# Performance work log

Hardware: AMD Instinct MI355X
Metric: run time of the kernel (lower is better)

The kernel has to match this reference:

```python
import jax, jax.numpy as jnp
import numpy as np

N_PATCHES = 256
PATCH = 16
D = 768
H = 12
DH = D // H
L = 12
OUT_D = 10
EPS = 1e-5


def _pos_embed(seq_len, d):
    i = np.arange(seq_len)[:, None].astype(np.float64)
    j = np.arange(d)[None, :].astype(np.float64)
    angle_even = i / 10000 ** (j / d)
    angle_odd = i / 10000 ** ((j - 1) / d)
    pe = np.where(np.arange(d)[None, :] % 2 == 0, np.sin(angle_even), np.cos(angle_odd))
    return jnp.asarray(pe, dtype=jnp.float32)


def _layernorm(x, g, b):
    mu = jnp.mean(x, axis=-1, keepdims=True)
    var = jnp.var(x, axis=-1, keepdims=True)
    return (x - mu) * jax.lax.rsqrt(var + EPS) * g + b


def setup_inputs() -> dict:
    key = jax.random.key(0)
    ks = jax.random.split(key, 16)
    s = 0.02
    return {
        "images": jax.random.normal(ks[0], (64, 1, N_PATCHES * PATCH), dtype=jnp.float32),
        "Wemb": jax.random.normal(ks[1], (D, PATCH), dtype=jnp.float32) * s,
        "bemb": jnp.zeros((D,), jnp.float32),
        "cls": jax.random.uniform(ks[2], (1, D), dtype=jnp.float32),
        "Wq": jax.random.normal(ks[3], (L, H, DH, DH), dtype=jnp.float32) * s,
        "bq": jnp.zeros((L, H, DH), jnp.float32),
        "Wk": jax.random.normal(ks[4], (L, H, DH, DH), dtype=jnp.float32) * s,
        "bk": jnp.zeros((L, H, DH), jnp.float32),
        "Wv": jax.random.normal(ks[5], (L, H, DH, DH), dtype=jnp.float32) * s,
        "bv": jnp.zeros((L, H, DH), jnp.float32),
        "ln1_g": jnp.ones((L, D), jnp.float32),
        "ln1_b": jnp.zeros((L, D), jnp.float32),
        "ln2_g": jnp.ones((L, D), jnp.float32),
        "ln2_b": jnp.zeros((L, D), jnp.float32),
        "W1": jax.random.normal(ks[6], (L, 4 * D, D), dtype=jnp.float32) * s,
        "b1": jnp.zeros((L, 4 * D), jnp.float32),
        "W2": jax.random.normal(ks[7], (L, D, 4 * D), dtype=jnp.float32) * s,
        "b2": jnp.zeros((L, D), jnp.float32),
        "Whead": jax.random.normal(ks[8], (OUT_D, D), dtype=jnp.float32) * s,
        "bhead": jnp.zeros((OUT_D,), jnp.float32),
    }


def reference(images, Wemb, bemb, cls, Wq, bq, Wk, bk, Wv, bv,
              ln1_g, ln1_b, ln2_g, ln2_b, W1, b1, W2, b2, Whead, bhead):
    n = images.shape[0]
    # patchify: (N,1,Lspec) -> (N, n_patches, patch_size)
    patches = images.reshape(n, N_PATCHES, PATCH)
    tok = jnp.einsum("npi,di->npd", patches, Wemb) + bemb  # linear embed
    tok = jnp.concatenate([jnp.broadcast_to(cls[None], (n, 1, D)), tok], axis=1)
    tok = tok + _pos_embed(N_PATCHES + 1, D)[None]  # (N, S, D), S = 257

    scale = 1.0 / jnp.sqrt(jnp.float32(DH))
    for l in range(L):
        x = tok
        h = _layernorm(x, ln1_g[l], ln1_b[l]).reshape(n, -1, H, DH)
        q = jnp.einsum("nshd,hod->nsho", h, Wq[l]) + bq[l][None, None]
        k = jnp.einsum("nshd,hod->nsho", h, Wk[l]) + bk[l][None, None]
        v = jnp.einsum("nshd,hod->nsho", h, Wv[l]) + bv[l][None, None]
        att = jax.nn.softmax(jnp.einsum("nqho,nkho->nhqk", q, k) * scale, axis=-1)
        o = jnp.einsum("nhqk,nkho->nqho", att, v).reshape(n, -1, D)
        x = x + o  # residual (no output projection in original MSA)
        h2 = _layernorm(x, ln2_g[l], ln2_b[l])
        mlp = jax.nn.gelu(jnp.einsum("nsd,fd->nsf", h2, W1[l]) + b1[l], approximate=False)
        tok = x + jnp.einsum("nsf,df->nsd", mlp, W2[l]) + b2[l]

    logits = tok[:, 0] @ Whead.T + bhead
    return jax.nn.softmax(logits, axis=-1)
```

## Files before the change

kernel.cpp:

```cpp
#include <hip/hip_runtime.h>
#include <math.h>
#include <stdint.h>

#define N_IMG 64
#define S_LEN 257
#define D_MODEL 768
#define H_HEADS 12
#define L_LAYERS 12
#define F_HID 3072
#define OUT_DIM 10
#define R_ROWS (N_IMG * S_LEN)
#define R_PAD 16640
#define SKV 320

typedef unsigned short ushort_t;
typedef __attribute__((ext_vector_type(4))) float f32x4;
typedef __attribute__((ext_vector_type(8))) short short8;
typedef __attribute__((ext_vector_type(2))) unsigned int u32x2;

__device__ __forceinline__ ushort_t f2bf(float x) {
    unsigned u = __float_as_uint(x);
    u += 0x7fffu + ((u >> 16) & 1u);
    return (ushort_t)(u >> 16);
}
__device__ __forceinline__ unsigned pack2(float a, float b) {
    return (unsigned)f2bf(a) | ((unsigned)f2bf(b) << 16);
}

__device__ __forceinline__ void glds16(const ushort_t* g, const ushort_t* l) {
    __builtin_amdgcn_global_load_lds(
        (const __attribute__((address_space(1))) unsigned int*)(uintptr_t)g,
        (__attribute__((address_space(3))) unsigned int*)(uintptr_t)l,
        16, 0, 0);
}

__global__ __launch_bounds__(256) void pos_kernel(float* __restrict__ pos) {
    int i = blockIdx.x;
    int t = threadIdx.x;
    for (int u = 0; u < 3; ++u) {
        int j = t + 256 * u;
        double e = (double)(j & ~1) / 768.0;
        double angle = (double)i * exp(-e * 9.210340371976184);
        double v = (j & 1) ? cos(angle) : sin(angle);
        pos[i * 768 + j] = (float)v;
    }
}

__global__ __launch_bounds__(256) void embed_kernel(const float* __restrict__ images,
                                                    const float* __restrict__ Wemb,
                                                    const float* __restrict__ bemb,
                                                    const float* __restrict__ cls,
                                                    const float* __restrict__ pos,
                                                    float* __restrict__ tok) {
    int b = blockIdx.x;
    int n = b / S_LEN, s = b % S_LEN;
    int t = threadIdx.x;
    __shared__ float p[16];
    if (s > 0 && t < 16) p[t] = images[n * 4096 + (s - 1) * 16 + t];
    __syncthreads();
    for (int u = 0; u < 3; ++u) {
        int d = t + 256 * u;
        float acc;
        if (s == 0) {
            acc = cls[d];
        } else {
            acc = bemb[d];
            const float4* w = (const float4*)(Wemb + d * 16);
            float4 w0 = w[0], w1 = w[1], w2 = w[2], w3 = w[3];
            acc += p[0] * w0.x + p[1] * w0.y + p[2] * w0.z + p[3] * w0.w;
            acc += p[4] * w1.x + p[5] * w1.y + p[6] * w1.z + p[7] * w1.w;
            acc += p[8] * w2.x + p[9] * w2.y + p[10] * w2.z + p[11] * w2.w;
            acc += p[12] * w3.x + p[13] * w3.y + p[14] * w3.z + p[15] * w3.w;
        }
        tok[(size_t)b * 768 + d] = acc + pos[s * 768 + d];
    }
}

__global__ __launch_bounds__(256) void ln_kernel(const float* __restrict__ x,
                                                 const float* __restrict__ g,
                                                 const float* __restrict__ b,
                                                 ushort_t* __restrict__ y) {
    int row = blockIdx.x * 4 + (threadIdx.x >> 6);
    int lane = threadIdx.x & 63;
    const float* xr = x + (size_t)row * 768 + lane * 4;
    float4 a0 = *(const float4*)xr;
    float4 a1 = *(const float4*)(xr + 256);
    float4 a2 = *(const float4*)(xr + 512);
    float s = (a0.x + a0.y + a0.z + a0.w) + (a1.x + a1.y + a1.z + a1.w) + (a2.x + a2.y + a2.z + a2.w);
    float sq = a0.x*a0.x + a0.y*a0.y + a0.z*a0.z + a0.w*a0.w
             + a1.x*a1.x + a1.y*a1.y + a1.z*a1.z + a1.w*a1.w
             + a2.x*a2.x + a2.y*a2.y + a2.z*a2.z + a2.w*a2.w;
    for (int o = 32; o; o >>= 1) {
        s += __shfl_xor(s, o);
        sq += __shfl_xor(sq, o);
    }
    float mu = s * (1.0f / 768.0f);
    float var = sq * (1.0f / 768.0f) - mu * mu;
    float rs = rsqrtf(var + 1e-5f);
    ushort_t* yr = y + (size_t)row * 768 + lane * 4;
#pragma unroll
    for (int i = 0; i < 3; ++i) {
        float4 av = (i == 0) ? a0 : (i == 1) ? a1 : a2;
        const float4 gg = *(const float4*)(g + lane * 4 + i * 256);
        const float4 bb = *(const float4*)(b + lane * 4 + i * 256);
        float o0 = (av.x - mu) * rs * gg.x + bb.x;
        float o1 = (av.y - mu) * rs * gg.y + bb.y;
        float o2 = (av.z - mu) * rs * gg.z + bb.z;
        float o3 = (av.w - mu) * rs * gg.w + bb.w;
        *(u32x2*)(yr + i * 256) = (u32x2){pack2(o0, o1), pack2(o2, o3)};
    }
}

__global__ __launch_bounds__(256) void conv_layer(const float* __restrict__ Wq,
                                                  const float* __restrict__ Wk,
                                                  const float* __restrict__ Wv,
                                                  const float* __restrict__ W1l,
                                                  const float* __restrict__ W2l,
                                                  ushort_t* __restrict__ wqkvbf,
                                                  ushort_t* __restrict__ w1bf,
                                                  ushort_t* __restrict__ w2bf) {
    const int NQKV = H_HEADS * 192 * 64;
    const int NW = F_HID * D_MODEL;
    int idx = (blockIdx.x * 256 + threadIdx.x) * 4;
    if (idx < NQKV) {
        int h = idx / (192 * 64);
        int rem = idx - h * 192 * 64;
        int o3 = rem >> 6, d = rem & 63;
        const float* src;
        int o;
        if (o3 < 64)       { src = Wq; o = o3; }
        else if (o3 < 128) { src = Wk; o = o3 - 64; }
        else               { src = Wv; o = o3 - 128; }
        float4 v = *(const float4*)(src + ((size_t)(h * 64 + o)) * 64 + d);
        *(u32x2*)(wqkvbf + idx) = (u32x2){pack2(v.x, v.y), pack2(v.z, v.w)};
    } else if (idx < NQKV + NW) {
        int i = idx - NQKV;
        float4 v = *(const float4*)(W1l + i);
        *(u32x2*)(w1bf + i) = (u32x2){pack2(v.x, v.y), pack2(v.z, v.w)};
    } else {
        int i = idx - NQKV - NW;
        float4 v = *(const float4*)(W2l + i);
        *(u32x2*)(w2bf + i) = (u32x2){pack2(v.x, v.y), pack2(v.z, v.w)};
    }
}

__global__ __launch_bounds__(256) void qkv_mfma(const ushort_t* __restrict__ xbf,
                                                const ushort_t* __restrict__ wqkv,
                                                const float* __restrict__ bq,
                                                const float* __restrict__ bk,
                                                const float* __restrict__ bv,
                                                ushort_t* __restrict__ qhb,
                                                ushort_t* __restrict__ khb,
                                                ushort_t* __restrict__ vtb) {
    __shared__ ushort_t As[128 * 64];
    int rt = blockIdx.x;
    int h = blockIdx.y;
    int t = threadIdx.x, lane = t & 63, wid = t >> 6;
    int wr = wid >> 1, wc = wid & 1;
    {
        int lr = t >> 3, lg = t & 7;
#pragma unroll
        for (int u = 0; u < 4; ++u) {
            int r = u * 32 + lr;
            int grow = rt * 128 + r;
            if (grow >= R_ROWS) grow = R_ROWS - 1;
            short8 a = *(const short8*)(xbf + (size_t)grow * 768 + h * 64 + lg * 8);
            *(short8*)&As[r * 64 + (lg ^ (r & 7)) * 8] = a;
        }
    }
    __syncthreads();
    int frow = lane & 15, g = lane >> 4;
    const ushort_t* wb = wqkv + (size_t)h * (192 * 64);
    f32x4 acc[4][6];
#pragma unroll
    for (int m = 0; m < 4; ++m)
#pragma unroll
        for (int n = 0; n < 6; ++n) acc[m][n] = (f32x4){0.f, 0.f, 0.f, 0.f};
#pragma unroll
    for (int kk = 0; kk < 2; ++kk) {
        short8 af[4], bfr[6];
#pragma unroll
        for (int m = 0; m < 4; ++m) {
            int r = wr * 64 + m * 16 + frow;
            af[m] = *(const short8*)&As[r * 64 + ((kk * 4 + g) ^ (r & 7)) * 8];
        }
#pragma unroll
        for (int n = 0; n < 6; ++n)
            bfr[n] = *(const short8*)(wb + (size_t)(wc * 96 + n * 16 + frow) * 64 + kk * 32 + g * 8);
#pragma unroll
        for (int m = 0; m < 4; ++m)
#pragma unroll
            for (int n = 0; n < 6; ++n)
                acc[m][n] = __builtin_amdgcn_mfma_f32_16x16x32_bf16(bfr[n], af[m], acc[m][n], 0, 0, 0);
    }
#pragma unroll
    for (int m = 0; m < 4; ++m) {
        int token = rt * 128 + wr * 64 + m * 16 + frow;
        if (token < R_ROWS) {
            unsigned nimg = (unsigned)token / 257u;
            unsigned s = (unsigned)token - nimg * 257u;
            size_t qk_base = ((size_t)(nimg * H_HEADS + h) * 257 + s) * 64;
            size_t v_base = (size_t)(nimg * H_HEADS + h) * (64 * SKV);
#pragma unroll
            for (int n = 0; n < 6; ++n) {
                int c = wc * 96 + n * 16 + g * 4;
                f32x4 a = acc[m][n];
                if (c < 64) {
                    const float4 bb = *(const float4*)(bq + h * 64 + c);
                    *(u32x2*)(qhb + qk_base + c) = (u32x2){
                        pack2((a[0] + bb.x) * 0.125f, (a[1] + bb.y) * 0.125f),
                        pack2((a[2] + bb.z) * 0.125f, (a[3] + bb.w) * 0.125f)};
                } else if (c < 128) {
                    const float4 bb = *(const float4*)(bk + h * 64 + (c - 64));
                    *(u32x2*)(khb + qk_base + (c - 64)) = (u32x2){
                        pack2(a[0] + bb.x, a[1] + bb.y), pack2(a[2] + bb.z, a[3] + bb.w)};
                } else {
                    const float4 bb = *(const float4*)(bv + h * 64 + (c - 128));
                    vtb[v_base + (size_t)(c - 128 + 0) * SKV + s] = f2bf(a[0] + bb.x);
                    vtb[v_base + (size_t)(c - 128 + 1) * SKV + s] = f2bf(a[1] + bb.y);
                    vtb[v_base + (size_t)(c - 128 + 2) * SKV + s] = f2bf(a[2] + bb.z);
                    vtb[v_base + (size_t)(c - 128 + 3) * SKV + s] = f2bf(a[3] + bb.w);
                }
            }
        }
    }
}

template <int NST>
__global__ __launch_bounds__(256) void attn_mfma(const ushort_t* __restrict__ qh,
                                                 const ushort_t* __restrict__ kh,
                                                 const ushort_t* __restrict__ vT,
                                                 float* __restrict__ tok, int base) {
    __shared__ ushort_t Plds[4][NST][1024];
    int nh = blockIdx.x;
    int h = nh % H_HEADS, n = nh / H_HEADS;
    int t = threadIdx.x, w = t >> 6, lane = t & 63;
    int lq = lane & 15, g = lane >> 4;
    const size_t hoff = ((size_t)n * H_HEADS + h) * (S_LEN * 64);
    const ushort_t* qhp = qh + hoff;
    const ushort_t* khp = kh + hoff;
    const ushort_t* vp  = vT + ((size_t)n * H_HEADS + h) * (64 * SKV);
    const int xorm = (lq & 7) << 4;

    short8 qf[NST][2];
    int qr0[NST];
    float m[NST], lsum[NST];
    f32x4 o[NST][4];
#pragma unroll
    for (int s = 0; s < NST; ++s) {
        int qrow = base + s * 64 + w * 16 + lq;
        qr0[s] = qrow;
        int qcl = qrow > 256 ? 256 : qrow;
#pragma unroll
        for (int kk = 0; kk < 2; ++kk)
            qf[s][kk] = *(const short8*)(qhp + (size_t)qcl * 64 + kk * 32 + g * 8);
        m[s] = -INFINITY; lsum[s] = 0.f;
#pragma unroll
        for (int dt = 0; dt < 4; ++dt) o[s][dt] = (f32x4){0.f, 0.f, 0.f, 0.f};
    }

    for (int kt = 0; kt < 5; ++kt) {
        short8 ah[4][2];
#pragma unroll
        for (int st = 0; st < 4; ++st) {
            int key = kt * 64 + st * 16 + lq;
            int kcl = key > 256 ? 256 : key;
            const ushort_t* krh = khp + (size_t)kcl * 64 + g * 8;
            ah[st][0] = *(const short8*)krh;
            ah[st][1] = *(const short8*)(krh + 32);
        }
        f32x4 c[NST][4];
#pragma unroll
        for (int s = 0; s < NST; ++s)
#pragma unroll
            for (int st = 0; st < 4; ++st) {
                c[s][st] = (f32x4){0.f, 0.f, 0.f, 0.f};
#pragma unroll
                for (int kk = 0; kk < 2; ++kk)
                    c[s][st] = __builtin_amdgcn_mfma_f32_16x16x32_bf16(ah[st][kk], qf[s][kk], c[s][st], 0, 0, 0);
            }
        float scale[NST];
        unsigned pw[NST][4][2];
#pragma unroll
        for (int s = 0; s < NST; ++s) {
            float tmax = -INFINITY;
#pragma unroll
            for (int st = 0; st < 4; ++st)
#pragma unroll
                for (int j = 0; j < 4; ++j) {
                    int key = kt * 64 + st * 16 + g * 4 + j;
                    float sv = (key <= 256) ? c[s][st][j] : -INFINITY;
                    c[s][st][j] = sv;
                    tmax = fmaxf(tmax, sv);
                }
            tmax = fmaxf(tmax, __shfl_xor(tmax, 16));
            tmax = fmaxf(tmax, __shfl_xor(tmax, 32));
            float mn = fmaxf(m[s], tmax);
            scale[s] = __expf(m[s] - mn);
            float psum = 0.f;
#pragma unroll
            for (int st = 0; st < 4; ++st) {
                float p0 = __expf(c[s][st][0] - mn), p1 = __expf(c[s][st][1] - mn);
                float p2 = __expf(c[s][st][2] - mn), p3 = __expf(c[s][st][3] - mn);
                psum += (p0 + p1) + (p2 + p3);
                pw[s][st][0] = pack2(p0, p1);
                pw[s][st][1] = pack2(p2, p3);
            }
            psum += __shfl_xor(psum, 16);
            psum += __shfl_xor(psum, 32);
            lsum[s] = lsum[s] * scale[s] + psum;
            m[s] = mn;
        }
#pragma unroll
        for (int s = 0; s < NST; ++s) {
            char* pwave = (char*)&Plds[w][s][0];
#pragma unroll
            for (int st = 0; st < 4; ++st) {
                int off = (lq * 128 + st * 32 + g * 8) ^ xorm;
                *(u32x2*)(pwave + off) = (u32x2){pw[s][st][0], pw[s][st][1]};
            }
#pragma unroll
            for (int dt = 0; dt < 4; ++dt) {
                o[s][dt][0] *= scale[s]; o[s][dt][1] *= scale[s];
                o[s][dt][2] *= scale[s]; o[s][dt][3] *= scale[s];
            }
        }
#pragma unroll
        for (int kk = 0; kk < 2; ++kk) {
            short8 pf[NST];
#pragma unroll
            for (int s = 0; s < NST; ++s) {
                int roff = (lq * 128 + kk * 64 + g * 16) ^ xorm;
                pf[s] = *(const short8*)((char*)&Plds[w][s][0] + roff);
            }
#pragma unroll
            for (int dt = 0; dt < 4; ++dt) {
                short8 vf = *(const short8*)(vp + (size_t)(dt * 16 + lq) * SKV + kt * 64 + kk * 32 + g * 8);
#pragma unroll
                for (int s = 0; s < NST; ++s)
                    o[s][dt] = __builtin_amdgcn_mfma_f32_16x16x32_bf16(vf, pf[s], o[s][dt], 0, 0, 0);
            }
        }
    }
#pragma unroll
    for (int s = 0; s < NST; ++s) {
        if (qr0[s] < S_LEN) {
            float inv = 1.0f / lsum[s];
            float* trow = tok + ((size_t)n * S_LEN + qr0[s]) * 768 + h * 64 + g * 4;
#pragma unroll
            for (int dt = 0; dt < 4; ++dt) {
                float4 old = *(const float4*)(trow + dt * 16);
                old.x += o[s][dt][0] * inv;
                old.y += o[s][dt][1] * inv;
                old.z += o[s][dt][2] * inv;
                old.w += o[s][dt][3] * inv;
                *(float4*)(trow + dt * 16) = old;
            }
        }
    }
}

__device__ __forceinline__ float gelu_fast(float x) {
    float s = fabsf(x) * 0.70710678118654752f;
    float t = 1.0f / (1.0f + 0.3275911f * s);
    float y = t * (0.254829592f + t * (-0.284496736f + t * (1.421413741f +
              t * (-1.453152027f + t * 1.061405429f))));
    float erfa = 1.0f - y * __expf(-s * s);
    float erfv = copysignf(erfa, x);
    return 0.5f * x * (1.0f + erfv);
}

template <int MODE>
__global__ __launch_bounds__(512, 2) void mfma_gemm(const ushort_t* __restrict__ A,
                                                    const ushort_t* __restrict__ B,
                                                    const float* __restrict__ bias,
                                                    void* __restrict__ Cv,
                                                    int K, int lda, int ldb, int ldc, int nbn) {
    __shared__ ushort_t As[4][256 * 32];
    __shared__ ushort_t Bs[4][256 * 32];
    int nwg = gridDim.x;
    int orig = blockIdx.x;
    int xcd = orig & 7, idx = orig >> 3;
    int q8 = nwg >> 3, r8 = nwg & 7;
    int cbase = (xcd < r8) ? xcd * (q8 + 1) : r8 * (q8 + 1) + (xcd - r8) * q8;
    int swz = cbase + idx;
    int bm = swz / nbn, bn = swz - bm * nbn;

    int t = threadIdx.x;
    int lane = t & 63, w = t >> 6;
    int wr = w >> 2, wc = w & 3;
    const ushort_t* Ag = A + (size_t)(bm * 256) * lda;
    const ushort_t* Bg = B + (size_t)(bn * 256) * ldb;
    int frow = lane & 15, g = lane >> 4;
    int srow = lane >> 2;
    int scol = ((lane & 3) ^ ((lane >> 3) & 3)) * 8;
    int rslot = (frow >> 1) & 3;

    f32x4 acc[8][4];
#pragma unroll
    for (int m = 0; m < 8; ++m)
#pragma unroll
        for (int n = 0; n < 4; ++n) acc[m][n] = (f32x4){0.f, 0.f, 0.f, 0.f};

    auto STAGE = [&](int buf, int kt) {
        int k0 = kt * 32;
#pragma unroll
        for (int i = 0; i < 2; ++i) {
            int rbase = w * 32 + i * 16;
            glds16(Ag + (size_t)(rbase + srow) * lda + k0 + scol, &As[buf][rbase * 32]);
            glds16(Bg + (size_t)(rbase + srow) * ldb + k0 + scol, &Bs[buf][rbase * 32]);
        }
    };
    STAGE(0, 0);
    STAGE(1, 1);
    STAGE(2, 2);
    int nt = K >> 5;
    for (int it = 0; it < nt; ++it) {
        int ahead = nt - 1 - it;
        if (ahead >= 2)      asm volatile("s_waitcnt vmcnt(8)" ::: "memory");
        else if (ahead == 1) asm volatile("s_waitcnt vmcnt(4)" ::: "memory");
        else                 asm volatile("s_waitcnt vmcnt(0)" ::: "memory");
        asm volatile("s_barrier" ::: "memory");
        if (it + 3 < nt) STAGE((it + 3) & 3, it + 3);
        const ushort_t* Ab = &As[it & 3][0];
        const ushort_t* Bb = &Bs[it & 3][0];
        short8 af[8], bf[4];
#pragma unroll
        for (int m = 0; m < 8; ++m) {
            int r = wr * 128 + m * 16 + frow;
            af[m] = *(const short8*)&Ab[r * 32 + ((g ^ rslot) * 8)];
        }
#pragma unroll
        for (int n = 0; n < 4; ++n) {
            int r = wc * 64 + n * 16 + frow;
            bf[n] = *(const short8*)&Bb[r * 32 + ((g ^ rslot) * 8)];
        }
#pragma unroll
        for (int m = 0; m < 8; ++m)
#pragma unroll
            for (int n = 0; n < 4; ++n)
                acc[m][n] = __builtin_amdgcn_mfma_f32_16x16x32_bf16(bf[n], af[m], acc[m][n], 0, 0, 0);
    }
    int row0 = bm * 256 + wr * 128 + frow;
    int col0 = bn * 256 + wc * 64 + g * 4;
#pragma unroll
    for (int n = 0; n < 4; ++n) {
        int col = col0 + n * 16;
        float4 bb = {0.f, 0.f, 0.f, 0.f};
        if (bias) bb = *(const float4*)(bias + col);
#pragma unroll
        for (int m = 0; m < 8; ++m) {
            int row = row0 + m * 16;
            f32x4 a = acc[m][n];
            float v0 = a[0] + bb.x, v1 = a[1] + bb.y, v2 = a[2] + bb.z, v3 = a[3] + bb.w;
            if (MODE == 0) {
                v0 = gelu_fast(v0); v1 = gelu_fast(v1); v2 = gelu_fast(v2); v3 = gelu_fast(v3);
                *(u32x2*)((ushort_t*)Cv + (size_t)row * ldc + col) =
                    (u32x2){pack2(v0, v1), pack2(v2, v3)};
            } else {
                float* cp = (float*)Cv + (size_t)row * ldc + col;
                float4 old = *(const float4*)cp;
                old.x += v0; old.y += v1; old.z += v2; old.w += v3;
                *(float4*)cp = old;
            }
        }
    }
}

__global__ __launch_bounds__(64) void head_kernel(const float* __restrict__ tok,
                                                  const float* __restrict__ Whead,
                                                  const float* __restrict__ bhead,
                                                  float* __restrict__ out) {
    int n = blockIdx.x;
    int t = threadIdx.x;
    __shared__ float logits[OUT_DIM];
    if (t < OUT_DIM) {
        float acc = bhead[t];
        const float* xr = tok + (size_t)n * S_LEN * 768;
        const float* w = Whead + t * 768;
        for (int d = 0; d < 768; ++d) acc += xr[d] * w[d];
        logits[t] = acc;
    }
    __syncthreads();
    if (t == 0) {
        float m = -INFINITY;
        for (int o = 0; o < OUT_DIM; ++o) m = fmaxf(m, logits[o]);
        float ssum = 0.f;
        float e[OUT_DIM];
        for (int o = 0; o < OUT_DIM; ++o) { e[o] = expf(logits[o] - m); ssum += e[o]; }
        float inv = 1.0f / ssum;
        for (int o = 0; o < OUT_DIM; ++o) out[n * OUT_DIM + o] = e[o] * inv;
    }
}

extern "C" void kernel_launch(void* const* d_in, const int* in_sizes, int n_in,
                              void* d_out, int out_size, void* d_ws, size_t ws_size,
                              hipStream_t stream) {
    const float* images = (const float*)d_in[0];
    const float* Wemb   = (const float*)d_in[1];
    const float* bemb   = (const float*)d_in[2];
    const float* cls    = (const float*)d_in[3];
    const float* Wq     = (const float*)d_in[4];
    const float* bq     = (const float*)d_in[5];
    const float* Wk     = (const float*)d_in[6];
    const float* bk     = (const float*)d_in[7];
    const float* Wv     = (const float*)d_in[8];
    const float* bv     = (const float*)d_in[9];
    const float* ln1_g  = (const float*)d_in[10];
    const float* ln1_b  = (const float*)d_in[11];
    const float* ln2_g  = (const float*)d_in[12];
    const float* ln2_b  = (const float*)d_in[13];
    const float* W1     = (const float*)d_in[14];
    const float* b1     = (const float*)d_in[15];
    const float* W2     = (const float*)d_in[16];
    const float* b2     = (const float*)d_in[17];
    const float* Whead  = (const float*)d_in[18];
    const float* bhead  = (const float*)d_in[19];
    float* out = (float*)d_out;

    const size_t TOKP = (size_t)R_PAD * D_MODEL;
    const size_t QKSZ = (size_t)N_IMG * H_HEADS * S_LEN * 64;
    const size_t VTSZ = (size_t)N_IMG * H_HEADS * 64 * SKV;
    const size_t WSZ  = (size_t)F_HID * D_MODEL;
    float* ws   = (float*)d_ws;
    float* pos  = ws;
    float* tok  = pos + 197376;
    ushort_t* xbf  = (ushort_t*)(tok + TOKP);
    ushort_t* qhb  = xbf + TOKP;
    ushort_t* khb  = qhb + QKSZ;
    ushort_t* vtb  = khb + QKSZ;
    ushort_t* wqkvbf = vtb + VTSZ;
    ushort_t* w1bf = wqkvbf + H_HEADS * 192 * 64;
    ushort_t* w2bf = w1bf + WSZ;
    ushort_t* hid_full = w2bf + WSZ;

    const size_t hid_bytes = (size_t)R_PAD * F_HID * 2;
    const size_t needed = ((char*)hid_full - (char*)d_ws) + hid_bytes;
    int nchunk = (ws_size >= needed) ? 1 : 2;
    int FC = F_HID / nchunk;
    ushort_t* hid = (nchunk == 1) ? hid_full : qhb;

    pos_kernel<<<S_LEN, 256, 0, stream>>>(pos);
    embed_kernel<<<R_ROWS, 256, 0, stream>>>(images, Wemb, bemb, cls, pos, tok);

    for (int l = 0; l < L_LAYERS; ++l) {
        const size_t wqkv_off = (size_t)l * H_HEADS * 64 * 64;
        const size_t bqkv_off = (size_t)l * H_HEADS * 64;
        ln_kernel<<<R_ROWS / 4, 256, 0, stream>>>(tok, ln1_g + l * 768, ln1_b + l * 768, xbf);
        conv_layer<<<4752, 256, 0, stream>>>(
            Wq + wqkv_off, Wk + wqkv_off, Wv + wqkv_off,
            W1 + (size_t)l * WSZ, W2 + (size_t)l * WSZ,
            wqkvbf, w1bf, w2bf);
        qkv_mfma<<<dim3(16512 / 128, H_HEADS), 256, 0, stream>>>(
            xbf, wqkvbf, bq + bqkv_off, bk + bqkv_off, bv + bqkv_off, qhb, khb, vtb);
        attn_mfma<2><<<N_IMG * H_HEADS, 256, 0, stream>>>(qhb, khb, vtb, tok, 0);
        attn_mfma<3><<<N_IMG * H_HEADS, 256, 0, stream>>>(qhb, khb, vtb, tok, 128);
        ln_kernel<<<R_ROWS / 4, 256, 0, stream>>>(tok, ln2_g + l * 768, ln2_b + l * 768, xbf);
        for (int c = 0; c < nchunk; ++c) {
            int c0 = c * FC;
            mfma_gemm<0><<<(FC / 256) * (R_PAD / 256), 512, 0, stream>>>(
                xbf, w1bf + (size_t)c0 * D_MODEL, b1 + (size_t)l * F_HID + c0, hid,
                768, 768, 768, FC, FC / 256);
            mfma_gemm<1><<<(D_MODEL / 256) * (R_PAD / 256), 512, 0, stream>>>(
                hid, w2bf + c0, (c == 0) ? (b2 + (size_t)l * D_MODEL) : (const float*)nullptr,
                tok, FC, FC, F_HID, D_MODEL, D_MODEL / 256);
        }
    }
    head_kernel<<<N_IMG, 64, 0, stream>>>(tok, Whead, bhead, out);
}
```

Baseline: 5.060 ms.

## Shrink MLP GEMM tiles to 128x128, trim row padding, fuse attention launches

The MLP GEMMs move from 256x256 tiles with 512 threads to 128x128 tiles with 256 threads. R_PAD drops to 16512, a multiple of 128, so fewer padded rows are computed. The two attention launches (query rows 0-127 and 128-256) are merged into one kernel that picks the half from the block index, saving a launch and letting both halves run concurrently. Smaller tiles give more blocks and better wave balance on the CUs, at the cost of less operand reuse per block.

```diff
diff --git a/kernel.cpp b/kernel.cpp
--- a/kernel.cpp
+++ b/kernel.cpp
@@ -10,7 +10,7 @@
 #define F_HID 3072
 #define OUT_DIM 10
 #define R_ROWS (N_IMG * S_LEN)
-#define R_PAD 16640
+#define R_PAD 16512
 #define SKV 320
 
 typedef unsigned short ushort_t;
@@ -227,20 +227,16 @@
 }
 
 template <int NST>
-__global__ __launch_bounds__(256) void attn_mfma(const ushort_t* __restrict__ qh,
-                                                 const ushort_t* __restrict__ kh,
-                                                 const ushort_t* __restrict__ vT,
-                                                 float* __restrict__ tok, int base) {
-    __shared__ ushort_t Plds[4][NST][1024];
-    int nh = blockIdx.x;
-    int h = nh % H_HEADS, n = nh / H_HEADS;
-    int t = threadIdx.x, w = t >> 6, lane = t & 63;
+__device__ __forceinline__ void attn_body(ushort_t* Pl,
+                                          const ushort_t* __restrict__ qhp,
+                                          const ushort_t* __restrict__ khp,
+                                          const ushort_t* __restrict__ vp,
+                                          float* __restrict__ tok,
+                                          int n, int h, int base, int t) {
+    int w = t >> 6, lane = t & 63;
     int lq = lane & 15, g = lane >> 4;
-    const size_t hoff = ((size_t)n * H_HEADS + h) * (S_LEN * 64);
-    const ushort_t* qhp = qh + hoff;
-    const ushort_t* khp = kh + hoff;
-    const ushort_t* vp  = vT + ((size_t)n * H_HEADS + h) * (64 * SKV);
     const int xorm = (lq & 7) << 4;
+    char* pw0 = (char*)(Pl + (size_t)w * 3 * 1024);
 
     short8 qf[NST][2];
     int qr0[NST];
@@ -313,7 +309,7 @@
         }
 #pragma unroll
         for (int s = 0; s < NST; ++s) {
-            char* pwave = (char*)&Plds[w][s][0];
+            char* pwave = pw0 + s * 2048;
 #pragma unroll
             for (int st = 0; st < 4; ++st) {
                 int off = (lq * 128 + st * 32 + g * 8) ^ xorm;
@@ -331,7 +327,7 @@
 #pragma unroll
             for (int s = 0; s < NST; ++s) {
                 int roff = (lq * 128 + kk * 64 + g * 16) ^ xorm;
-                pf[s] = *(const short8*)((char*)&Plds[w][s][0] + roff);
+                pf[s] = *(const short8*)(pw0 + s * 2048 + roff);
             }
 #pragma unroll
             for (int dt = 0; dt < 4; ++dt) {
@@ -358,6 +354,24 @@
             }
         }
     }
+}
+
+__global__ __launch_bounds__(256) void attn_fused(const ushort_t* __restrict__ qh,
+                                                  const ushort_t* __restrict__ kh,
+                                                  const ushort_t* __restrict__ vT,
+                                                  float* __restrict__ tok) {
+    __shared__ ushort_t Plds[4 * 3 * 1024];
+    int b = blockIdx.x;
+    int half = b & 1;
+    int nh = b >> 1;
+    int h = nh % H_HEADS, n = nh / H_HEADS;
+    const size_t hoff = ((size_t)n * H_HEADS + h) * (S_LEN * 64);
+    const ushort_t* qhp = qh + hoff;
+    const ushort_t* khp = kh + hoff;
+    const ushort_t* vp  = vT + ((size_t)n * H_HEADS + h) * (64 * SKV);
+    int t = threadIdx.x;
+    if (half == 0) attn_body<2>(Plds, qhp, khp, vp, tok, n, h, 0, t);
+    else           attn_body<3>(Plds, qhp, khp, vp, tok, n, h, 128, t);
 }
 
 __device__ __forceinline__ float gelu_fast(float x) {
@@ -371,34 +385,34 @@
 }
 
 template <int MODE>
-__global__ __launch_bounds__(512, 2) void mfma_gemm(const ushort_t* __restrict__ A,
-                                                    const ushort_t* __restrict__ B,
-                                                    const float* __restrict__ bias,
-                                                    void* __restrict__ Cv,
-                                                    int K, int lda, int ldb, int ldc, int nbn) {
-    __shared__ ushort_t As[4][256 * 32];
-    __shared__ ushort_t Bs[4][256 * 32];
+__global__ __launch_bounds__(256) void mfma_gemm(const ushort_t* __restrict__ A,
+                                                 const ushort_t* __restrict__ B,
+                                                 const float* __restrict__ bias,
+                                                 void* __restrict__ Cv,
+                                                 int K, int lda, int ldb, int ldc, int nbn) {
+    __shared__ ushort_t As[4][128 * 32];
+    __shared__ ushort_t Bs[4][128 * 32];
     int nwg = gridDim.x;
     int orig = blockIdx.x;
     int xcd = orig & 7, idx = orig >> 3;
     int q8 = nwg >> 3, r8 = nwg & 7;
     int cbase = (xcd < r8) ? xcd * (q8 + 1) : r8 * (q8 + 1) + (xcd - r8) * q8;
-    int swz = cbase + idx;
-    int bm = swz / nbn, bn = swz - bm * nbn;
+    int swb = cbase + idx;
+    int bm = swb / nbn, bn = swb - bm * nbn;
 
     int t = threadIdx.x;
     int lane = t & 63, w = t >> 6;
-    int wr = w >> 2, wc = w & 3;
-    const ushort_t* Ag = A + (size_t)(bm * 256) * lda;
-    const ushort_t* Bg = B + (size_t)(bn * 256) * ldb;
+    int wr = w >> 1, wc = w & 1;
+    const ushort_t* Ag = A + (size_t)(bm * 128) * lda;
+    const ushort_t* Bg = B + (size_t)(bn * 128) * ldb;
     int frow = lane & 15, g = lane >> 4;
     int srow = lane >> 2;
     int scol = ((lane & 3) ^ ((lane >> 3) & 3)) * 8;
     int rslot = (frow >> 1) & 3;
 
-    f32x4 acc[8][4];
-#pragma unroll
-    for (int m = 0; m < 8; ++m)
+    f32x4 acc[4][4];
+#pragma unroll
+    for (int m = 0; m < 4; ++m)
 #pragma unroll
         for (int n = 0; n < 4; ++n) acc[m][n] = (f32x4){0.f, 0.f, 0.f, 0.f};
 
@@ -406,7 +420,7 @@
         int k0 = kt * 32;
 #pragma unroll
         for (int i = 0; i < 2; ++i) {
-            int rbase = w * 32 + i * 16;
+            int rbase = i * 64 + w * 16;
             glds16(Ag + (size_t)(rbase + srow) * lda + k0 + scol, &As[buf][rbase * 32]);
             glds16(Bg + (size_t)(rbase + srow) * ldb + k0 + scol, &Bs[buf][rbase * 32]);
         }
@@ -424,10 +438,10 @@
         if (it + 3 < nt) STAGE((it + 3) & 3, it + 3);
         const ushort_t* Ab = &As[it & 3][0];
         const ushort_t* Bb = &Bs[it & 3][0];
-        short8 af[8], bf[4];
-#pragma unroll
-        for (int m = 0; m < 8; ++m) {
-            int r = wr * 128 + m * 16 + frow;
+        short8 af[4], bf[4];
+#pragma unroll
+        for (int m = 0; m < 4; ++m) {
+            int r = wr * 64 + m * 16 + frow;
             af[m] = *(const short8*)&Ab[r * 32 + ((g ^ rslot) * 8)];
         }
 #pragma unroll
@@ -436,21 +450,21 @@
             bf[n] = *(const short8*)&Bb[r * 32 + ((g ^ rslot) * 8)];
         }
 #pragma unroll
-        for (int m = 0; m < 8; ++m)
+        for (int m = 0; m < 4; ++m)
 #pragma unroll
             for (int n = 0; n < 4; ++n)
                 acc[m][n] = __builtin_amdgcn_mfma_f32_16x16x32_bf16(bf[n], af[m], acc[m][n], 0, 0, 0);
     }
-    int row0 = bm * 256 + wr * 128 + frow;
-    int col0 = bn * 256 + wc * 64 + g * 4;
-#pragma unroll
-    for (int n = 0; n < 4; ++n) {
-        int col = col0 + n * 16;
-        float4 bb = {0.f, 0.f, 0.f, 0.f};
-        if (bias) bb = *(const float4*)(bias + col);
-#pragma unroll
-        for (int m = 0; m < 8; ++m) {
-            int row = row0 + m * 16;
+    int row0 = bm * 128 + wr * 64 + frow;
+    int col0 = bn * 128 + wc * 64 + g * 4;
+#pragma unroll
+    for (int m = 0; m < 4; ++m) {
+        int row = row0 + m * 16;
+#pragma unroll
+        for (int n = 0; n < 4; ++n) {
+            int col = col0 + n * 16;
+            float4 bb = {0.f, 0.f, 0.f, 0.f};
+            if (bias) bb = *(const float4*)(bias + col);
             f32x4 a = acc[m][n];
             float v0 = a[0] + bb.x, v1 = a[1] + bb.y, v2 = a[2] + bb.z, v3 = a[3] + bb.w;
             if (MODE == 0) {
@@ -551,19 +565,18 @@
             Wq + wqkv_off, Wk + wqkv_off, Wv + wqkv_off,
             W1 + (size_t)l * WSZ, W2 + (size_t)l * WSZ,
             wqkvbf, w1bf, w2bf);
-        qkv_mfma<<<dim3(16512 / 128, H_HEADS), 256, 0, stream>>>(
+        qkv_mfma<<<dim3(R_PAD / 128, H_HEADS), 256, 0, stream>>>(
             xbf, wqkvbf, bq + bqkv_off, bk + bqkv_off, bv + bqkv_off, qhb, khb, vtb);
-        attn_mfma<2><<<N_IMG * H_HEADS, 256, 0, stream>>>(qhb, khb, vtb, tok, 0);
-        attn_mfma<3><<<N_IMG * H_HEADS, 256, 0, stream>>>(qhb, khb, vtb, tok, 128);
+        attn_fused<<<N_IMG * H_HEADS * 2, 256, 0, stream>>>(qhb, khb, vtb, tok);
         ln_kernel<<<R_ROWS / 4, 256, 0, stream>>>(tok, ln2_g + l * 768, ln2_b + l * 768, xbf);
         for (int c = 0; c < nchunk; ++c) {
             int c0 = c * FC;
-            mfma_gemm<0><<<(FC / 256) * (R_PAD / 256), 512, 0, stream>>>(
+            mfma_gemm<0><<<(FC / 128) * (R_PAD / 128), 256, 0, stream>>>(
                 xbf, w1bf + (size_t)c0 * D_MODEL, b1 + (size_t)l * F_HID + c0, hid,
-                768, 768, 768, FC, FC / 256);
-            mfma_gemm<1><<<(D_MODEL / 256) * (R_PAD / 256), 512, 0, stream>>>(
+                768, 768, 768, FC, FC / 128);
+            mfma_gemm<1><<<(D_MODEL / 128) * (R_PAD / 128), 256, 0, stream>>>(
                 hid, w2bf + c0, (c == 0) ? (b2 + (size_t)l * D_MODEL) : (const float*)nullptr,
-                tok, FC, FC, F_HID, D_MODEL, D_MODEL / 256);
+                tok, FC, FC, F_HID, D_MODEL, D_MODEL / 128);
         }
     }
     head_kernel<<<N_IMG, 64, 0, stream>>>(tok, Whead, bhead, out);
```

New measurement: 5.255 ms. +3.8%, slower.
